# Kernel optimization log

Hardware: AMD Instinct MI355X
Metric: run time of the kernel (lower is better)

The kernel has to match this reference:

```python
import jax, jax.numpy as jnp
import numpy as np

EPS = 1e-6
D = 1152          # hidden_size
NH_HEADS = 16     # num_attention_heads
HD = D // NH_HEADS
INTER = 4304      # intermediate_size
H4 = 4 * D        # 4608
I4 = 4 * INTER    # 17216
B, H, W = 8, 64, 64
WH, WW = 2, 2


def setup_inputs() -> dict:
    key = jax.random.key(0)
    ks = jax.random.split(key, 12)
    s = 0.02
    inp = {
        "hidden_states": jax.random.normal(ks[0], (B, H * W, D), jnp.float32),
        "tgt_sizes": jnp.full((B, 2), 64, dtype=jnp.int32),
        "attention_mask": jnp.zeros((B, 1, 1, H * W), jnp.float32),
        "ln1_g": jnp.ones((D,), jnp.float32),
        "ln1_b": jnp.zeros((D,), jnp.float32),
        "qkv_w": jax.random.normal(ks[1], (D, 3 * D), jnp.float32) * s,
        "qkv_b": jnp.zeros((3 * D,), jnp.float32),
        "out_w": jax.random.normal(ks[2], (D, D), jnp.float32) * s,
        "out_b": jnp.zeros((D,), jnp.float32),
        "pre_g": jnp.ones((H4,), jnp.float32),
        "pre_b": jnp.zeros((H4,), jnp.float32),
        "w1": jax.random.normal(ks[3], (H4, I4), jnp.float32) * s,
        "b1": jnp.zeros((I4,), jnp.float32),
        "w2": jax.random.normal(ks[4], (I4, D), jnp.float32) * s,
        "b2": jnp.zeros((D,), jnp.float32),
    }
    return inp


def _layernorm(x, g, b):
    m = x.mean(-1, keepdims=True)
    v = ((x - m) ** 2).mean(-1, keepdims=True)
    return (x - m) * jax.lax.rsqrt(v + EPS) * g + b


def _partition(x):
    # x: [B, H*W, D] -> windows [B, nh*nw, wh*ww, D]
    nh, nw = H // WH, W // WW
    x = x.reshape(B, nh, WH, nw, WW, D)
    x = x.transpose(0, 1, 3, 2, 4, 5)  # [B, nh, nw, wh, ww, D]
    return x.reshape(B, nh * nw, WH * WW, D)


def _unpartition(x):
    # windows [B, nh*nw, wh*ww, D] -> [B, H*W, D]
    nh, nw = H // WH, W // WW
    x = x.reshape(B, nh, nw, WH, WW, D)
    x = x.transpose(0, 1, 3, 2, 4, 5)  # [B, nh, wh, nw, ww, D]
    return x.reshape(B, H * W, D)


def reference(hidden_states, tgt_sizes, attention_mask, ln1_g, ln1_b,
              qkv_w, qkv_b, out_w, out_b, pre_g, pre_b, w1, b1, w2, b2):
    nh, nw = H // WH, W // WW
    nwin = nh * nw
    residual = hidden_states
    hs = _layernorm(hidden_states, ln1_g, ln1_b)

    # window self-attention over 4-token windows
    xw = _partition(hs).reshape(B * nwin, WH * WW, D)
    qkv = xw @ qkv_w + qkv_b                               # [N, 4, 3D]
    q, k, v = jnp.split(qkv, 3, axis=-1)
    q = q.reshape(-1, WH * WW, NH_HEADS, HD)
    k = k.reshape(-1, WH * WW, NH_HEADS, HD)
    v = v.reshape(-1, WH * WW, NH_HEADS, HD)
    scale = HD ** -0.5
    scores = jnp.einsum('nqhd,nkhd->nhqk', q, k) * scale
    probs = jax.nn.softmax(scores, axis=-1)
    o = jnp.einsum('nhqk,nkhd->nqhd', probs, v).reshape(-1, WH * WW, D)
    o = o @ out_w + out_b
    attn_out = _unpartition(o.reshape(B, nwin, WH * WW, D))
    hs = residual + attn_out                               # [B, H*W, D]

    # MLP downsample over 2x2 windows
    xw = _partition(hs)                                    # [B, nwin, 4, D]
    res = xw.mean(axis=2)                                  # [B, nwin, D]
    xf = xw.reshape(B, nwin, WH * WW * D)                  # [B, nwin, 4D]
    xf = _layernorm(xf, pre_g, pre_b)
    xf = jax.nn.gelu(xf @ w1 + b1, approximate=True)
    xf = xf @ w2 + b2
    new_hidden = xf + res                                  # [B, nwin, D]

    new_tgt_sizes = tgt_sizes // 2
    # all samples fully valid -> mask of zeros (no -inf positions)
    min_val = jnp.finfo(new_hidden.dtype).min
    valid = jnp.arange(nwin)[None, :] < (new_tgt_sizes[:, 0] * new_tgt_sizes[:, 1])[:, None]
    new_attention_mask = ((~valid).astype(new_hidden.dtype) * min_val)[:, None, None, :]
    return new_hidden, new_tgt_sizes, new_attention_mask
```

## Files before the change

kernel.cpp:

```cpp
#include <hip/hip_runtime.h>
#include <cstdint>
#include <cstddef>

#define DEV __device__ __forceinline__
typedef unsigned short u16;
typedef unsigned int u32;
typedef short bf16x8 __attribute__((ext_vector_type(8)));
typedef float f32x4 __attribute__((ext_vector_type(4)));

typedef __attribute__((address_space(1))) u32 GU32;
typedef __attribute__((address_space(3))) u32 LU32;

DEV float bf2f(u16 v){ u32 x = ((u32)v)<<16; float f; __builtin_memcpy(&f,&x,4); return f; }
DEV u16 f2bf(float f){ u32 x; __builtin_memcpy(&x,&f,4); return (u16)((x + 0x7fffu + ((x>>16)&1u)) >> 16); }

DEV int map_row(int r){
  int b = r>>12, rr = r&4095;
  int win = rr>>2, t = rr&3;
  int wy = win>>5, wx = win&31;
  int y = (wy<<1) + (t>>1), x = (wx<<1) + (t&1);
  return (b<<12) + (y<<6) + x;
}

DEV void gl_lds16(const void* g, void* l){
  __builtin_amdgcn_global_load_lds((const GU32*)g, (LU32*)l, 16, 0, 0);
}

DEV void block_red2(float& s, float& ss, float* red){
  #pragma unroll
  for (int o=32;o;o>>=1){ s += __shfl_down(s,o); ss += __shfl_down(ss,o); }
  const int wv = threadIdx.x>>6;
  if ((threadIdx.x&63)==0){ red[wv*2]=s; red[wv*2+1]=ss; }
  __syncthreads();
  s  = red[0]+red[2]+red[4]+red[6];
  ss = red[1]+red[3]+red[5]+red[7];
}

__launch_bounds__(256)
__global__ void tconv_k(const float* __restrict__ W, u16* __restrict__ WT, int K, int N){
  __shared__ float tl[64][65];
  const int n0 = blockIdx.x << 6, k0 = blockIdx.y << 6;
  const int tx = threadIdx.x & 63, ty = threadIdx.x >> 6;
  #pragma unroll
  for (int rr = 0; rr < 64; rr += 4)
    tl[rr+ty][tx] = W[(size_t)(k0+rr+ty)*N + (n0+tx)];
  __syncthreads();
  #pragma unroll
  for (int rr = 0; rr < 64; rr += 4)
    WT[(size_t)(n0+rr+ty)*K + (k0+tx)] = f2bf(tl[tx][rr+ty]);
}

__launch_bounds__(256)
__global__ void ln1_k(const float* __restrict__ X, const float* __restrict__ g,
                      const float* __restrict__ b, u16* __restrict__ Y){
  __shared__ float red[8];
  const int r = blockIdx.x;
  const float* xr = X + (size_t)map_row(r)*1152;
  const int tid = threadIdx.x;
  const bool has2 = tid < 32;
  float4 v0 = ((const float4*)xr)[tid];
  float4 v1 = {0,0,0,0};
  float s  = v0.x+v0.y+v0.z+v0.w;
  float ss = v0.x*v0.x+v0.y*v0.y+v0.z*v0.z+v0.w*v0.w;
  if (has2){
    v1 = ((const float4*)xr)[tid+256];
    s  += v1.x+v1.y+v1.z+v1.w;
    ss += v1.x*v1.x+v1.y*v1.y+v1.z*v1.z+v1.w*v1.w;
  }
  block_red2(s, ss, red);
  const float mean = s*(1.0f/1152.0f);
  const float rstd = rsqrtf(ss*(1.0f/1152.0f) - mean*mean + 1e-6f);
  u16* yr = Y + (size_t)r*1152;
  {
    float4 gg = ((const float4*)g)[tid];
    float4 bb = ((const float4*)b)[tid];
    ushort4 o;
    o.x = f2bf((v0.x-mean)*rstd*gg.x + bb.x);
    o.y = f2bf((v0.y-mean)*rstd*gg.y + bb.y);
    o.z = f2bf((v0.z-mean)*rstd*gg.z + bb.z);
    o.w = f2bf((v0.w-mean)*rstd*gg.w + bb.w);
    *(ushort4*)(yr + tid*4) = o;
  }
  if (has2){
    float4 gg = ((const float4*)g)[tid+256];
    float4 bb = ((const float4*)b)[tid+256];
    ushort4 o;
    o.x = f2bf((v1.x-mean)*rstd*gg.x + bb.x);
    o.y = f2bf((v1.y-mean)*rstd*gg.y + bb.y);
    o.z = f2bf((v1.z-mean)*rstd*gg.z + bb.z);
    o.w = f2bf((v1.w-mean)*rstd*gg.w + bb.w);
    *(ushort4*)(yr + (tid+256)*4) = o;
  }
}

#define BAR()  asm volatile("s_barrier" ::: "memory")
#define LGKM0() do{ asm volatile("s_waitcnt lgkmcnt(0)" ::: "memory"); \
                    __builtin_amdgcn_sched_barrier(0); }while(0)
#define VMW8() asm volatile("s_waitcnt vmcnt(8)" ::: "memory")
#define VMW6() asm volatile("s_waitcnt vmcnt(6)" ::: "memory")
#define VMW4() asm volatile("s_waitcnt vmcnt(4)" ::: "memory")
#define VMW0() asm volatile("s_waitcnt vmcnt(0)" ::: "memory")
#define WNONE() do{}while(0)

template<int EPI>
__launch_bounds__(512, 1)
__global__ void gemm8p_k(const u16* __restrict__ A, const u16* __restrict__ BT,
                         int M, int N, int K, int lda, int ldb,
                         void* __restrict__ C, int ldc,
                         const float* __restrict__ bias,
                         const float* __restrict__ aux,
                         int nTM, int nTN)
{
  __shared__ __align__(16) u16 LS[2][2][2][8192];
  const int tid = threadIdx.x;
  const int lane = tid & 63;
  const int wave = tid >> 6;
  const int wr = wave >> 2, wc = wave & 3;

  const int bid  = blockIdx.x;
  const int band = 16 * nTN;
  const int bb   = bid / band, rr_ = bid % band;
  int mcnt = nTM - (bb<<4); if (mcnt > 16) mcnt = 16;
  const int mt = (bb<<4) + rr_ % mcnt;
  const int nt = rr_ / mcnt;
  const int m0 = mt << 8, n0 = nt << 8;

  const int lr1 = tid >> 3, sl = tid & 7;
  const int x_  = sl ^ (lr1 & 7);
  const int grow = ((x_ >> 2) << 7) + lr1;
  const int q_   = x_ & 3;
  const u16* aS = A  + (size_t)(m0 + grow)*lda + q_*8;
  const u16* bS = BT + (size_t)(n0 + grow)*ldb + q_*8;
  const size_t aR64 = (size_t)64*lda, bR64 = (size_t)64*ldb;

  const int l15 = lane & 15, l7 = lane & 7, qh = lane >> 4;
  const int aOff = l15*64 + ((((wr<<2)|qh) ^ l7) << 3);
  const int bOff = ((wc&1)<<12) + l15*64 + (((((wc>>1)<<2)|qh) ^ l7) << 3);

  f32x4 acc[8][4] = {};
  bf16x8 af[4], bv[4];
  const int NT = K >> 6;

#define ST(op_, db_, kh_, t_) do{ \
    const u16* src__ = (op_ ? bS : aS) + (size_t)(t_)*64 + (kh_)*32; \
    u16* dst__ = &LS[(db_)][(op_)][(kh_)][tid*8]; \
    gl_lds16(src__, dst__); \
    gl_lds16(src__ + (op_ ? bR64 : aR64), dst__ + 4096); \
  }while(0)

#define READA(base_, mh_) do{ \
    const u16* ap__ = (base_) + aOff + ((mh_)?4096:0); \
    _Pragma("unroll") for (int i__=0;i__<4;i__++) af[i__] = *(const bf16x8*)(ap__ + i__*1024); \
  }while(0)

#define READB(base_) do{ \
    const u16* bp__ = (base_) + bOff; \
    _Pragma("unroll") for (int i__=0;i__<4;i__++) bv[i__] = *(const bf16x8*)(bp__ + i__*1024); \
  }while(0)

#define MFMA16(B_) do{ \
    __builtin_amdgcn_s_setprio(1); \
    _Pragma("unroll") for (int i__=0;i__<4;i__++) \
      _Pragma("unroll") for (int n__=0;n__<4;n__++) \
        acc[(B_)+i__][n__] = __builtin_amdgcn_mfma_f32_16x16x32_bf16(af[i__], bv[n__], acc[(B_)+i__][n__], 0,0,0); \
    __builtin_amdgcn_s_setprio(0); \
  }while(0)

#define GROUP(t_, SE12, SE3, Wp1, Wp3) do{ \
    const int cb__ = (t_) & 1; \
    const u16* rA0__ = &LS[cb__][0][0][0]; \
    const u16* rB0__ = &LS[cb__][1][0][0]; \
    const u16* rA1__ = &LS[cb__][0][1][0]; \
    const u16* rB1__ = &LS[cb__][1][1][0]; \
     \
    READB(rB0__); READA(rA0__, 0); \
    BAR(); LGKM0(); MFMA16(0); \
     \
    READA(rA0__, 1); if (SE12) ST(0, cb__^1, 1, (t_)+1); \
    Wp1(); BAR(); LGKM0(); MFMA16(4); \
     \
    READB(rB1__); READA(rA1__, 0); if (SE12) ST(1, cb__^1, 1, (t_)+1); \
    BAR(); LGKM0(); MFMA16(0); \
     \
    READA(rA1__, 1); if (SE3) { ST(0, cb__, 0, (t_)+2); ST(1, cb__, 0, (t_)+2); } \
    Wp3(); BAR(); LGKM0(); MFMA16(4); \
  }while(0)

  ST(0,0,0,0); ST(1,0,0,0); ST(0,0,1,0); ST(1,0,1,0); ST(0,1,0,1); ST(1,1,0,1);
  VMW8(); BAR();

  int t = 0;
  for (; t < NT-2; ++t) GROUP(t, 1, 1, VMW6, VMW8);
  GROUP(t, 1, 0, VMW6, VMW4); ++t;
  GROUP(t, 0, 0, VMW0, WNONE);

#undef GROUP
#undef MFMA16
#undef READB
#undef READA
#undef ST

  #pragma unroll
  for (int mi=0;mi<8;mi++){
    const int row = m0 + (wr<<7) + (mi<<4) + ((lane>>4)<<2);
    #pragma unroll
    for (int ni=0;ni<4;ni++){
      const int col = n0 + (wc<<6) + (ni<<4) + (lane&15);
      if (col < N){
        const float bvv = bias[col];
        #pragma unroll
        for (int r2=0;r2<4;r2++){
          const int rw = row + r2;
          float v = acc[mi][ni][r2] + bvv;
          if (EPI==0){
            ((u16*)C)[(size_t)rw*ldc + col] = f2bf(v);
          } else if (EPI==1){
            v += aux[(size_t)map_row(rw)*ldc + col];
            ((u16*)C)[(size_t)rw*ldc + col] = f2bf(v);
          } else if (EPI==2){
            const float x = v;
            const float c = 0.7978845608028654f*(x + 0.044715f*x*x*x);
            v = 0.5f*x*(1.0f + tanhf(c));
            ((u16*)C)[(size_t)rw*ldc + col] = f2bf(v);
          } else {
            v += aux[(size_t)rw*ldc + col];
            ((float*)C)[(size_t)rw*ldc + col] = v;
          }
        }
      }
    }
  }
}

__launch_bounds__(256)
__global__ void attn_k(const u16* __restrict__ QKV, u16* __restrict__ O){
  const int wave = threadIdx.x >> 6, lane = threadIdx.x & 63;
  const int wg = blockIdx.x*4 + wave;
  const int t = lane >> 4, h = lane & 15;
  const u16* base = QKV + (size_t)wg*4*3456;

  float q[72];
  {
    const u16* qp = base + t*3456 + h*72;
    #pragma unroll
    for (int i=0;i<9;i++){
      bf16x8 v = *(const bf16x8*)(qp + i*8);
      #pragma unroll
      for (int j=0;j<8;j++) q[i*8+j] = bf2f((u16)v[j]);
    }
  }
  float sc[4];
  #pragma unroll
  for (int tp=0;tp<4;tp++){
    const u16* kp = base + tp*3456 + 1152 + h*72;
    float a = 0.f;
    #pragma unroll
    for (int i=0;i<9;i++){
      bf16x8 v = *(const bf16x8*)(kp + i*8);
      #pragma unroll
      for (int j=0;j<8;j++) a += q[i*8+j]*bf2f((u16)v[j]);
    }
    sc[tp] = a * 0.11785113019775793f;
  }
  const float mx = fmaxf(fmaxf(sc[0],sc[1]), fmaxf(sc[2],sc[3]));
  float p[4]; float sum = 0.f;
  #pragma unroll
  for (int tp=0;tp<4;tp++){ p[tp] = __expf(sc[tp]-mx); sum += p[tp]; }
  const float inv = 1.0f/sum;
  float o[72];
  #pragma unroll
  for (int i=0;i<72;i++) o[i] = 0.f;
  #pragma unroll
  for (int tp=0;tp<4;tp++){
    const float w = p[tp]*inv;
    const u16* vp = base + tp*3456 + 2304 + h*72;
    #pragma unroll
    for (int i=0;i<9;i++){
      bf16x8 v = *(const bf16x8*)(vp + i*8);
      #pragma unroll
      for (int j=0;j<8;j++) o[i*8+j] += w*bf2f((u16)v[j]);
    }
  }
  u16* op = O + (size_t)(wg*4+t)*1152 + h*72;
  #pragma unroll
  for (int i=0;i<9;i++){
    bf16x8 sv;
    #pragma unroll
    for (int j=0;j<8;j++) sv[j] = (short)f2bf(o[i*8+j]);
    *(bf16x8*)(op + i*8) = sv;
  }
}

__launch_bounds__(256)
__global__ void ln2res_k(const u16* __restrict__ hs2, const float* __restrict__ g,
                         const float* __restrict__ b, u16* __restrict__ Y,
                         float* __restrict__ res){
  __shared__ float buf[4608];
  __shared__ float red[8];
  const int w = blockIdx.x;
  const u16* xr = hs2 + (size_t)w*4608;
  float s = 0.f, ss = 0.f;
  for (int i = threadIdx.x*8; i < 4608; i += 2048){
    bf16x8 v = *(const bf16x8*)(xr + i);
    #pragma unroll
    for (int j=0;j<8;j++){
      float f = bf2f((u16)v[j]);
      buf[i+j] = f; s += f; ss += f*f;
    }
  }
  block_red2(s, ss, red);
  const float mean = s*(1.0f/4608.0f);
  const float rstd = rsqrtf(ss*(1.0f/4608.0f) - mean*mean + 1e-6f);
  u16* yr = Y + (size_t)w*4608;
  for (int i = threadIdx.x*8; i < 4608; i += 2048){
    bf16x8 sv;
    #pragma unroll
    for (int j=0;j<8;j++)
      sv[j] = (short)f2bf((buf[i+j]-mean)*rstd*g[i+j] + b[i+j]);
    *(bf16x8*)(yr + i) = sv;
  }
  for (int d = threadIdx.x; d < 1152; d += 256)
    res[(size_t)w*1152 + d] = 0.25f*(buf[d]+buf[d+1152]+buf[d+2304]+buf[d+3456]);
}

__global__ void tail_k(const int* __restrict__ tgt, float* __restrict__ out){
  const int tid = blockIdx.x*blockDim.x + threadIdx.x;
  float* t_out = out + 9437184;
  float* m_out = t_out + 16;
  if (tid < 16) t_out[tid] = (float)(tgt[tid] / 2);
  for (int i = tid; i < 8192; i += 256*32){
    const int b = i >> 10, w = i & 1023;
    const int lim = (tgt[b*2]/2) * (tgt[b*2+1]/2);
    m_out[i] = (w < lim) ? 0.0f : -3.40282346638528859812e+38f;
  }
}

extern "C" void kernel_launch(void* const* d_in, const int* in_sizes, int n_in,
                              void* d_out, int out_size, void* d_ws, size_t ws_size,
                              hipStream_t stream){
  const float* hidden = (const float*)d_in[0];
  const int*   tgt    = (const int*)  d_in[1];
  const float* ln1_g  = (const float*)d_in[3];
  const float* ln1_b  = (const float*)d_in[4];
  const float* qkv_w  = (const float*)d_in[5];
  const float* qkv_b  = (const float*)d_in[6];
  const float* out_w  = (const float*)d_in[7];
  const float* out_b  = (const float*)d_in[8];
  const float* pre_g  = (const float*)d_in[9];
  const float* pre_b  = (const float*)d_in[10];
  const float* w1     = (const float*)d_in[11];
  const float* b1     = (const float*)d_in[12];
  const float* w2     = (const float*)d_in[13];
  const float* b2     = (const float*)d_in[14];
  float* out = (float*)d_out;

  char* p = (char*)d_ws;
  auto alloc = [&](size_t bytes)->void*{ void* r = p; p += (bytes + 255) & ~(size_t)255; return r; };
  u16* w1T = (u16*)alloc(17216ull*4608*2);
  u16* w2T = (u16*)alloc(1152ull*17216*2);
  u16* wqT = (u16*)alloc(3456ull*1152*2);
  u16* woT = (u16*)alloc(1152ull*1152*2);
  u16* Xln = (u16*)alloc(32768ull*1152*2);
  char* qr = (char*)alloc(32768ull*3456*2);
  u16*   QKV  = (u16*)qr;
  u16*   hs2  = (u16*)qr;
  float* res  = (float*)(qr + 75497472);
  u16*   xfln = (u16*)(qr + 150994944);
  u16*   h1   = Xln;

  tconv_k<<<dim3(17216/64, 4608/64), 256, 0, stream>>>(w1, w1T, 4608, 17216);
  tconv_k<<<dim3(1152/64, 17216/64), 256, 0, stream>>>(w2, w2T, 17216, 1152);
  tconv_k<<<dim3(3456/64, 1152/64), 256, 0, stream>>>(qkv_w, wqT, 1152, 3456);
  tconv_k<<<dim3(1152/64, 1152/64), 256, 0, stream>>>(out_w, woT, 1152, 1152);
  ln1_k<<<32768, 256, 0, stream>>>(hidden, ln1_g, ln1_b, Xln);
  gemm8p_k<0><<<dim3(128*14), 512, 0, stream>>>(Xln, wqT, 32768, 3456, 1152, 1152, 1152,
                                                QKV, 3456, qkv_b, nullptr, 128, 14);
  attn_k<<<2048, 256, 0, stream>>>(QKV, Xln);
  gemm8p_k<1><<<dim3(128*5), 512, 0, stream>>>(Xln, woT, 32768, 1152, 1152, 1152, 1152,
                                               hs2, 1152, out_b, hidden, 128, 5);
  ln2res_k<<<8192, 256, 0, stream>>>(hs2, pre_g, pre_b, xfln, res);
  for (int r0 = 0; r0 < 8192; r0 += 4352){
    const int m = (8192 - r0 < 4352) ? (8192 - r0) : 4352;
    gemm8p_k<2><<<dim3((m>>8)*68), 512, 0, stream>>>(xfln + (size_t)r0*4608, w1T,
                                                     m, 17216, 4608, 4608, 4608,
                                                     h1, 17216, b1, nullptr, m>>8, 68);
    gemm8p_k<3><<<dim3((m>>8)*5), 512, 0, stream>>>(h1, w2T,
                                                    m, 1152, 17216, 17216, 17216,
                                                    out + (size_t)r0*1152, 1152, b2,
                                                    res + (size_t)r0*1152, m>>8, 5);
  }
  tail_k<<<32, 256, 0, stream>>>(tgt, out);
}
```

Baseline: 2.824 ms.

## Use smaller-tile GEMM for MLP down-projection and split rows into two chunks

Adds a simpler 128x128-tile, 256-thread GEMM kernel with two blocks per CU and uses it for the w2 down-projection (N=1152, K=17216). It replaces the 256-row pipelined kernel that launched only a few hundred workgroups. The row chunk changes from 4352 to 4096 so both chunks are the same size. The goal is more workgroups and better CU occupancy for the narrow-N GEMM, but the new kernel has no double buffering or software pipelining, so global loads are not overlapped with MFMA work.

```diff
diff --git a/kernel.cpp b/kernel.cpp
--- a/kernel.cpp
+++ b/kernel.cpp
@@ -172,16 +172,12 @@
     const u16* rB0__ = &LS[cb__][1][0][0]; \
     const u16* rA1__ = &LS[cb__][0][1][0]; \
     const u16* rB1__ = &LS[cb__][1][1][0]; \
-     \
     READB(rB0__); READA(rA0__, 0); \
     BAR(); LGKM0(); MFMA16(0); \
-     \
     READA(rA0__, 1); if (SE12) ST(0, cb__^1, 1, (t_)+1); \
     Wp1(); BAR(); LGKM0(); MFMA16(4); \
-     \
     READB(rB1__); READA(rA1__, 0); if (SE12) ST(1, cb__^1, 1, (t_)+1); \
     BAR(); LGKM0(); MFMA16(0); \
-     \
     READA(rA1__, 1); if (SE3) { ST(0, cb__, 0, (t_)+2); ST(1, cb__, 0, (t_)+2); } \
     Wp3(); BAR(); LGKM0(); MFMA16(4); \
   }while(0)
@@ -232,6 +228,90 @@
   }
 }
 
+template<int EPI>
+__launch_bounds__(256,2)
+__global__ void gemm_k(const u16* __restrict__ A, const u16* __restrict__ BT,
+                       int M, int N, int K, int lda,
+                       void* __restrict__ C, int ldc,
+                       const float* __restrict__ bias,
+                       const float* __restrict__ aux,
+                       int row_off)
+{
+  __shared__ __align__(16) u16 As[128*64];
+  __shared__ __align__(16) u16 Bs[128*64];
+  const int tid = threadIdx.x;
+  const int lane = tid & 63;
+  const int wave = tid >> 6;
+  const int wr = wave >> 1, wc = wave & 1;
+  const int m0 = blockIdx.y << 7, n0 = blockIdx.x << 7;
+
+  f32x4 acc[4][4] = {};
+
+  const int srow = tid >> 3;
+  const int scol = (tid & 7) << 3;
+  const u16* Ab = A  + (size_t)(m0 + srow)*lda + scol;
+  const u16* Bb = BT + (size_t)(n0 + srow)*K   + scol;
+
+  for (int kt = 0; kt < K; kt += 64) {
+    #pragma unroll
+    for (int i=0;i<4;i++)
+      gl_lds16(Ab + kt + (size_t)(i*32)*lda, &As[(size_t)(i*256+tid)*8]);
+    #pragma unroll
+    for (int i=0;i<4;i++)
+      gl_lds16(Bb + kt + (size_t)(i*32)*K, &Bs[(size_t)(i*256+tid)*8]);
+    __syncthreads();
+    #pragma unroll
+    for (int kk=0; kk<64; kk+=32) {
+      bf16x8 af[4], bv[4];
+      const int ko = kk + ((lane>>4)<<3);
+      #pragma unroll
+      for (int mi=0;mi<4;mi++)
+        af[mi] = *(const bf16x8*)&As[(((wr<<6)+(mi<<4)+(lane&15))<<6) + ko];
+      #pragma unroll
+      for (int ni=0;ni<4;ni++)
+        bv[ni] = *(const bf16x8*)&Bs[(((wc<<6)+(ni<<4)+(lane&15))<<6) + ko];
+      #pragma unroll
+      for (int mi=0;mi<4;mi++)
+        #pragma unroll
+        for (int ni=0;ni<4;ni++)
+          acc[mi][ni] = __builtin_amdgcn_mfma_f32_16x16x32_bf16(af[mi], bv[ni], acc[mi][ni], 0,0,0);
+    }
+    __syncthreads();
+  }
+
+  #pragma unroll
+  for (int mi=0;mi<4;mi++){
+    const int rbase = m0 + (wr<<6) + (mi<<4) + ((lane>>4)<<2);
+    #pragma unroll
+    for (int ni=0;ni<4;ni++){
+      const int col = n0 + (wc<<6) + (ni<<4) + (lane&15);
+      if (col < N) {
+        const float bvv = bias[col];
+        #pragma unroll
+        for (int r2=0;r2<4;r2++){
+          const int row = rbase + r2;
+          float v = acc[mi][ni][r2] + bvv;
+          if (EPI==0){
+            ((u16*)C)[(size_t)row*ldc + col] = f2bf(v);
+          } else if (EPI==1){
+            const int src = map_row(row + row_off);
+            v += aux[(size_t)src*ldc + col];
+            ((u16*)C)[(size_t)row*ldc + col] = f2bf(v);
+          } else if (EPI==2){
+            const float x = v;
+            const float c = 0.7978845608028654f*(x + 0.044715f*x*x*x);
+            v = 0.5f*x*(1.0f + tanhf(c));
+            ((u16*)C)[(size_t)row*ldc + col] = f2bf(v);
+          } else {
+            v += aux[(size_t)row*ldc + col];
+            ((float*)C)[(size_t)row*ldc + col] = v;
+          }
+        }
+      }
+    }
+  }
+}
+
 __launch_bounds__(256)
 __global__ void attn_k(const u16* __restrict__ QKV, u16* __restrict__ O){
   const int wave = threadIdx.x >> 6, lane = threadIdx.x & 63;
@@ -379,15 +459,15 @@
   gemm8p_k<1><<<dim3(128*5), 512, 0, stream>>>(Xln, woT, 32768, 1152, 1152, 1152, 1152,
                                                hs2, 1152, out_b, hidden, 128, 5);
   ln2res_k<<<8192, 256, 0, stream>>>(hs2, pre_g, pre_b, xfln, res);
-  for (int r0 = 0; r0 < 8192; r0 += 4352){
-    const int m = (8192 - r0 < 4352) ? (8192 - r0) : 4352;
+  for (int r0 = 0; r0 < 8192; r0 += 4096){
+    const int m = 4096;
     gemm8p_k<2><<<dim3((m>>8)*68), 512, 0, stream>>>(xfln + (size_t)r0*4608, w1T,
                                                      m, 17216, 4608, 4608, 4608,
                                                      h1, 17216, b1, nullptr, m>>8, 68);
-    gemm8p_k<3><<<dim3((m>>8)*5), 512, 0, stream>>>(h1, w2T,
-                                                    m, 1152, 17216, 17216, 17216,
-                                                    out + (size_t)r0*1152, 1152, b2,
-                                                    res + (size_t)r0*1152, m>>8, 5);
+    gemm_k<3><<<dim3(9, m>>7), 256, 0, stream>>>(h1, w2T,
+                                                 m, 1152, 17216, 17216,
+                                                 out + (size_t)r0*1152, 1152, b2,
+                                                 res + (size_t)r0*1152, 0);
   }
   tail_k<<<32, 256, 0, stream>>>(tgt, out);
 }
```

Result: slower. 2.931 ms (+3.8%).
